# Kernel tuning notes

Hardware: AMD Instinct MI355X
Metric: run time of the kernel (lower is better)

The kernel has to match this reference:

```python
import jax, jax.numpy as jnp
import numpy as np

NODES, NFEAT = 128, 256


def setup_inputs() -> dict:
    key = jax.random.key(0)
    k1, k2, k3, k4, k5, k6 = jax.random.split(key, 6)
    B = 512
    x = jax.random.normal(k1, (B, NODES, NFEAT), dtype=jnp.float32)
    adj = jax.random.uniform(k2, (B, NODES, NODES), dtype=jnp.float32)
    # GraphConvolution(nfeat, nfeat): weight [nfeat, nfeat], bias [nfeat]
    s = 1.0 / np.sqrt(NFEAT)
    gcn_w = jax.random.uniform(k3, (NFEAT, NFEAT), minval=-s, maxval=s, dtype=jnp.float32)
    gcn_b = jax.random.uniform(k4, (NFEAT,), minval=-s, maxval=s, dtype=jnp.float32)
    # fc: Linear(nfeat*nodes, nfeat), torch layout [out, in]
    s2 = 1.0 / np.sqrt(NFEAT * NODES)
    fc_w = jax.random.uniform(k5, (NFEAT, NFEAT * NODES), minval=-s2, maxval=s2, dtype=jnp.float32)
    fc_b = jax.random.uniform(k6, (NFEAT,), minval=-s2, maxval=s2, dtype=jnp.float32)
    return {"x": x, "adj": adj, "gcn_w": gcn_w, "gcn_b": gcn_b, "fc_w": fc_w, "fc_b": fc_b}


def reference(x, adj, gcn_w, gcn_b, fc_w, fc_b):
    B = x.shape[0]
    # Per-sample loop GCN fused as batched matmuls:
    # support = X @ W ; out = A @ support + b
    support = jnp.einsum('bnf,fg->bng', x, gcn_w)          # [B, nodes, nfeat]
    mid = jnp.einsum('bnm,bmg->bng', adj, support) + gcn_b  # [B, nodes, nfeat]
    # cat along dim0 then reshape(-1, nfeat*nodes) == per-graph flatten
    flat = mid.reshape(B, NODES * NFEAT)
    output = flat @ fc_w.T + fc_b                           # [B, nfeat]
    useful_input = x[:, 0, :]                               # [B, nfeat]
    return (output, useful_input, output)
```

## Files before the change

kernel.cpp:

```cpp
#include <hip/hip_runtime.h>

#define NODES 128
#define NFEAT 256
#define BATCH 512
#define KTOT  (NODES * NFEAT)
#define SPLIT 64
#define KCH   (KTOT / SPLIT)

typedef __bf16 bf16_t;
typedef bf16_t bf16x4 __attribute__((ext_vector_type(4)));
typedef bf16_t bf16x8 __attribute__((ext_vector_type(8)));
typedef float  f32x4  __attribute__((ext_vector_type(4)));

#define BK    32
#define LDK   40
#define BK2   64
#define LDK2  72
#define TILE  128
#define GT    64

__device__ __forceinline__ void bar() {
    asm volatile("s_waitcnt lgkmcnt(0)\n\ts_barrier" ::: "memory");
}

__device__ __forceinline__ bf16x8 cvt8(const float4 a, const float4 b) {
    bf16x8 t;
    t[0] = (bf16_t)a.x; t[1] = (bf16_t)a.y; t[2] = (bf16_t)a.z; t[3] = (bf16_t)a.w;
    t[4] = (bf16_t)b.x; t[5] = (bf16_t)b.y; t[6] = (bf16_t)b.z; t[7] = (bf16_t)b.w;
    return t;
}

struct XT { float4 v[4]; };
__device__ __forceinline__ void xload(const float* __restrict__ src, int ld, int k0,
                                      int tid, XT& t) {
#pragma unroll
    for (int i = 0; i < 2; i++) {
        int f = tid + i * 256, r = f >> 2, c = f & 3;
        t.v[2 * i]     = *(const float4*)(src + (size_t)r * ld + k0 + c * 8);
        t.v[2 * i + 1] = *(const float4*)(src + (size_t)r * ld + k0 + c * 8 + 4);
    }
}
__device__ __forceinline__ void xstore(bf16_t* __restrict__ dst, int tid, const XT& t) {
#pragma unroll
    for (int i = 0; i < 2; i++) {
        int f = tid + i * 256, r = f >> 2, c = f & 3;
        *(bf16x8*)(dst + r * LDK + c * 8) = cvt8(t.v[2 * i], t.v[2 * i + 1]);
    }
}

struct XT2 { float4 v[8]; };
__device__ __forceinline__ void xload2(const float* __restrict__ src, int ld, int k0,
                                       int tid, XT2& t) {
#pragma unroll
    for (int i = 0; i < 4; i++) {
        int f = tid + i * 256, r = f >> 3, c = f & 7;
        t.v[2 * i]     = *(const float4*)(src + (size_t)r * ld + k0 + c * 8);
        t.v[2 * i + 1] = *(const float4*)(src + (size_t)r * ld + k0 + c * 8 + 4);
    }
}
__device__ __forceinline__ void xstore2(bf16_t* __restrict__ dst, int tid, const XT2& t) {
#pragma unroll
    for (int i = 0; i < 4; i++) {
        int f = tid + i * 256, r = f >> 3, c = f & 7;
        *(bf16x8*)(dst + r * LDK2 + c * 8) = cvt8(t.v[2 * i], t.v[2 * i + 1]);
    }
}

struct AT2 { bf16x8 v[4]; };
__device__ __forceinline__ void aload2(const bf16_t* __restrict__ src, int ld, int k0,
                                       int tid, AT2& t) {
#pragma unroll
    for (int i = 0; i < 4; i++) {
        int f = tid + i * 256, r = f >> 3, c = f & 7;
        t.v[i] = *(const bf16x8*)(src + (size_t)r * ld + k0 + c * 8);
    }
}
__device__ __forceinline__ void astore2(bf16_t* __restrict__ dst, int tid, const AT2& t) {
#pragma unroll
    for (int i = 0; i < 4; i++) {
        int f = tid + i * 256, r = f >> 3, c = f & 7;
        *(bf16x8*)(dst + r * LDK2 + c * 8) = t.v[i];
    }
}

__global__ __launch_bounds__(256)
void k_wt(const float* __restrict__ w, bf16_t* __restrict__ wT) {
    const int g0 = blockIdx.x * 4;
    const int k  = threadIdx.x;
    const float4 v = *(const float4*)(w + (size_t)k * NFEAT + g0);
    wT[(size_t)(g0 + 0) * NFEAT + k] = (bf16_t)v.x;
    wT[(size_t)(g0 + 1) * NFEAT + k] = (bf16_t)v.y;
    wT[(size_t)(g0 + 2) * NFEAT + k] = (bf16_t)v.z;
    wT[(size_t)(g0 + 3) * NFEAT + k] = (bf16_t)v.w;
}

__global__ __launch_bounds__(256)
void k_fwt(const float* __restrict__ w, bf16_t* __restrict__ wb) {
    const size_t i = ((size_t)blockIdx.x * 256 + threadIdx.x) * 8;
    const float4 a = *(const float4*)(w + i);
    const float4 b = *(const float4*)(w + i + 4);
    *(bf16x8*)(wb + i) = cvt8(a, b);
}

__global__ __launch_bounds__(256, 4)
void k_fused12(const float* __restrict__ x, const float* __restrict__ adj,
               const bf16_t* __restrict__ wT, const float* __restrict__ gcn_b,
               bf16_t* __restrict__ mid) {
    __shared__ __align__(16) bf16_t As[2][TILE * LDK];
    __shared__ __align__(16) bf16_t Sb[GT * 128];
    const int id  = blockIdx.y * 4 + blockIdx.x;
    const int xcd = id & 7, jj = id >> 3;
    const int b   = (xcd << 6) | (jj >> 2);
    const int n0  = (jj & 3) * GT;
    const int tid = threadIdx.x;
    const int lane = tid & 63, w = tid >> 6, wm = w & 1, wn = w >> 1;
    const int l15 = lane & 15, q = lane >> 4;
    const float* xb   = x   + (size_t)b * NODES * NFEAT;
    const float* adjb = adj + (size_t)b * NODES * NODES;

    const bf16_t* wrow[2];
#pragma unroll
    for (int j = 0; j < 2; j++)
        wrow[j] = wT + (size_t)(n0 + wn * 32 + j * 16 + l15) * NFEAT + q * 8;

    f32x4 acc[4][2] = {};
    {
        XT r[3];
        xload(xb, NFEAT, 0 * BK, tid, r[0]);
        xload(xb, NFEAT, 1 * BK, tid, r[1]);
        xload(xb, NFEAT, 2 * BK, tid, r[2]);
        xstore(As[0], tid, r[0]);
        bar();
#pragma unroll
        for (int k = 0; k < 8; k++) {
            if (k + 3 < 8) xload(xb, NFEAT, (k + 3) * BK, tid, r[k % 3]);
            bf16x8 bcur[2];
#pragma unroll
            for (int j = 0; j < 2; j++) bcur[j] = *(const bf16x8*)(wrow[j] + k * BK);
            bf16x8 a[4];
#pragma unroll
            for (int i = 0; i < 4; i++)
                a[i] = *(const bf16x8*)(&As[k & 1][(wm * 64 + i * 16 + l15) * LDK + q * 8]);
#pragma unroll
            for (int i = 0; i < 4; i++)
#pragma unroll
                for (int j = 0; j < 2; j++)
                    acc[i][j] = __builtin_amdgcn_mfma_f32_16x16x32_bf16(a[i], bcur[j], acc[i][j], 0, 0, 0);
            if (k + 1 < 8) xstore(As[(k + 1) & 1], tid, r[(k + 1) % 3]);
            bar();
        }
    }

    XT r[3];
    xload(adjb, NODES, 0 * BK, tid, r[0]);
    xload(adjb, NODES, 1 * BK, tid, r[1]);
    xload(adjb, NODES, 2 * BK, tid, r[2]);
#pragma unroll
    for (int i = 0; i < 4; i++)
#pragma unroll
        for (int j = 0; j < 2; j++)
#pragma unroll
            for (int rr = 0; rr < 4; rr++) {
                int m = wm * 64 + i * 16 + q * 4 + rr;
                int g = wn * 32 + j * 16 + l15;
                int slot = (m >> 3) ^ (g & 15);
                Sb[g * 128 + slot * 8 + (m & 7)] = (bf16_t)acc[i][j][rr];
            }
    bar();
    xstore(As[0], tid, r[0]);
    bar();

    f32x4 acc2[4][2] = {};
#pragma unroll
    for (int k = 0; k < 4; k++) {
        if (k + 3 < 4) xload(adjb, NODES, (k + 3) * BK, tid, r[k % 3]);
        bf16x8 a[4], bb[2];
#pragma unroll
        for (int i = 0; i < 4; i++)
            a[i] = *(const bf16x8*)(&As[k & 1][(wm * 64 + i * 16 + l15) * LDK + q * 8]);
#pragma unroll
        for (int j = 0; j < 2; j++) {
            int R = wn * 32 + j * 16 + l15;
            int slot = (k * 4 + q) ^ (R & 15);
            bb[j] = *(const bf16x8*)(&Sb[R * 128 + slot * 8]);
        }
#pragma unroll
        for (int i = 0; i < 4; i++)
#pragma unroll
            for (int j = 0; j < 2; j++)
                acc2[i][j] = __builtin_amdgcn_mfma_f32_16x16x32_bf16(a[i], bb[j], acc2[i][j], 0, 0, 0);
        if (k + 1 < 4) xstore(As[(k + 1) & 1], tid, r[(k + 1) % 3]);
        bar();
    }
    bf16_t* outb = mid + (size_t)b * NODES * NFEAT;
#pragma unroll
    for (int j = 0; j < 2; j++) {
        int g = n0 + wn * 32 + j * 16 + l15;
        float bias = gcn_b[g];
#pragma unroll
        for (int i = 0; i < 4; i++)
#pragma unroll
            for (int rr = 0; rr < 4; rr++) {
                int node = wm * 64 + i * 16 + q * 4 + rr;
                outb[(size_t)node * NFEAT + g] = (bf16_t)(acc2[i][j][rr] + bias);
            }
    }
}

__global__ __launch_bounds__(256, 2)
void k_out_bf(const bf16_t* __restrict__ flat, const bf16_t* __restrict__ fcwb,
              bf16_t* __restrict__ part) {
    __shared__ __align__(16) bf16_t As[2][TILE * LDK2];
    __shared__ __align__(16) bf16_t Bs[2][TILE * LDK2];
    const int m0 = blockIdx.x * TILE;
    const int n0 = blockIdx.y * TILE;
    const int kb = blockIdx.z * KCH;
    const int tid = threadIdx.x;
    const int lane = tid & 63, w = tid >> 6, wm = w & 1, wn = w >> 1;
    const int l15 = lane & 15, q = lane >> 4;
    f32x4 acc[4][4] = {};
    const bf16_t* fa = flat + (size_t)m0 * KTOT;
    const bf16_t* fb = fcwb + (size_t)n0 * KTOT;

    AT2 ra[3], rb[2];
    aload2(fa, KTOT, kb + 0 * BK2, tid, ra[0]);
    aload2(fb, KTOT, kb + 0 * BK2, tid, rb[0]);
    aload2(fa, KTOT, kb + 1 * BK2, tid, ra[1]);
    aload2(fb, KTOT, kb + 1 * BK2, tid, rb[1]);
    aload2(fa, KTOT, kb + 2 * BK2, tid, ra[2]);
    astore2(As[0], tid, ra[0]);
    astore2(Bs[0], tid, rb[0]);
    bar();
#pragma unroll
    for (int k = 0; k < 8; k++) {
        if (k + 3 < 8) aload2(fa, KTOT, kb + (k + 3) * BK2, tid, ra[k % 3]);
        if (k + 2 < 8) aload2(fb, KTOT, kb + (k + 2) * BK2, tid, rb[k & 1]);
#pragma unroll
        for (int kk = 0; kk < BK2; kk += BK) {
            bf16x8 a[4], bbf[4];
#pragma unroll
            for (int i = 0; i < 4; i++)
                a[i] = *(const bf16x8*)(&As[k & 1][(wm * 64 + i * 16 + l15) * LDK2 + kk + q * 8]);
#pragma unroll
            for (int j = 0; j < 4; j++)
                bbf[j] = *(const bf16x8*)(&Bs[k & 1][(wn * 64 + j * 16 + l15) * LDK2 + kk + q * 8]);
#pragma unroll
            for (int i = 0; i < 4; i++)
#pragma unroll
                for (int j = 0; j < 4; j++)
                    acc[i][j] = __builtin_amdgcn_mfma_f32_16x16x32_bf16(a[i], bbf[j], acc[i][j], 0, 0, 0);
        }
        if (k + 1 < 8) {
            astore2(As[(k + 1) & 1], tid, ra[(k + 1) % 3]);
            astore2(Bs[(k + 1) & 1], tid, rb[(k + 1) & 1]);
        }
        bar();
    }
    bf16_t* pb = part + (size_t)blockIdx.z * BATCH * NFEAT;
#pragma unroll
    for (int i = 0; i < 4; i++)
#pragma unroll
        for (int j = 0; j < 4; j++)
#pragma unroll
            for (int r = 0; r < 4; r++) {
                int bt_ = m0 + wm * 64 + i * 16 + q * 4 + r;
                int o   = n0 + wn * 64 + j * 16 + l15;
                pb[(size_t)bt_ * NFEAT + o] = (bf16_t)acc[i][j][r];
            }
}

__global__ __launch_bounds__(256, 2)
void k_out(const bf16_t* __restrict__ flat, const float* __restrict__ fcw,
           bf16_t* __restrict__ part) {
    __shared__ __align__(16) bf16_t As[2][TILE * LDK2];
    __shared__ __align__(16) bf16_t Bs[2][TILE * LDK2];
    const int m0 = blockIdx.x * TILE;
    const int n0 = blockIdx.y * TILE;
    const int kb = blockIdx.z * KCH;
    const int tid = threadIdx.x;
    const int lane = tid & 63, w = tid >> 6, wm = w & 1, wn = w >> 1;
    const int l15 = lane & 15, q = lane >> 4;
    f32x4 acc[4][4] = {};
    const bf16_t* fa = flat + (size_t)m0 * KTOT;
    const float*  fb = fcw + (size_t)n0 * KTOT;

    AT2 ra[3]; XT2 rb[2];
    aload2(fa, KTOT, kb + 0 * BK2, tid, ra[0]);
    xload2(fb, KTOT, kb + 0 * BK2, tid, rb[0]);
    aload2(fa, KTOT, kb + 1 * BK2, tid, ra[1]);
    xload2(fb, KTOT, kb + 1 * BK2, tid, rb[1]);
    aload2(fa, KTOT, kb + 2 * BK2, tid, ra[2]);
    astore2(As[0], tid, ra[0]);
    xstore2(Bs[0], tid, rb[0]);
    bar();
#pragma unroll
    for (int k = 0; k < 8; k++) {
        if (k + 3 < 8) aload2(fa, KTOT, kb + (k + 3) * BK2, tid, ra[k % 3]);
        if (k + 2 < 8) xload2(fb, KTOT, kb + (k + 2) * BK2, tid, rb[k & 1]);
#pragma unroll
        for (int kk = 0; kk < BK2; kk += BK) {
            bf16x8 a[4], bbf[4];
#pragma unroll
            for (int i = 0; i < 4; i++)
                a[i] = *(const bf16x8*)(&As[k & 1][(wm * 64 + i * 16 + l15) * LDK2 + kk + q * 8]);
#pragma unroll
            for (int j = 0; j < 4; j++)
                bbf[j] = *(const bf16x8*)(&Bs[k & 1][(wn * 64 + j * 16 + l15) * LDK2 + kk + q * 8]);
#pragma unroll
            for (int i = 0; i < 4; i++)
#pragma unroll
                for (int j = 0; j < 4; j++)
                    acc[i][j] = __builtin_amdgcn_mfma_f32_16x16x32_bf16(a[i], bbf[j], acc[i][j], 0, 0, 0);
        }
        if (k + 1 < 8) {
            astore2(As[(k + 1) & 1], tid, ra[(k + 1) % 3]);
            xstore2(Bs[(k + 1) & 1], tid, rb[(k + 1) & 1]);
        }
        bar();
    }
    bf16_t* pb = part + (size_t)blockIdx.z * BATCH * NFEAT;
#pragma unroll
    for (int i = 0; i < 4; i++)
#pragma unroll
        for (int j = 0; j < 4; j++)
#pragma unroll
            for (int r = 0; r < 4; r++) {
                int bt_ = m0 + wm * 64 + i * 16 + q * 4 + r;
                int o   = n0 + wn * 64 + j * 16 + l15;
                pb[(size_t)bt_ * NFEAT + o] = (bf16_t)acc[i][j][r];
            }
}

__global__ __launch_bounds__(256)
void k_reduce(const bf16_t* __restrict__ part, const float* __restrict__ fc_b,
              const float* __restrict__ x, float* __restrict__ out) {
    const int g4 = (blockIdx.x * 256 + threadIdx.x) * 4;
    const int o = g4 & (NFEAT - 1), b = g4 >> 8;
    float s[4];
    const float4 c0 = *(const float4*)(fc_b + o);
    s[0] = c0.x; s[1] = c0.y; s[2] = c0.z; s[3] = c0.w;
#pragma unroll 8
    for (int i = 0; i < SPLIT; i++) {
        bf16x4 p = *(const bf16x4*)(part + (size_t)i * BATCH * NFEAT + g4);
#pragma unroll
        for (int j = 0; j < 4; j++) s[j] += (float)p[j];
    }
    float4 o0 = make_float4(s[0], s[1], s[2], s[3]);
    *(float4*)(out + g4) = o0;
    *(float4*)(out + 2 * BATCH * NFEAT + g4) = o0;
    *(float4*)(out + BATCH * NFEAT + g4) = *(const float4*)(x + (size_t)b * NODES * NFEAT + o);
}

extern "C" void kernel_launch(void* const* d_in, const int* in_sizes, int n_in,
                              void* d_out, int out_size, void* d_ws, size_t ws_size,
                              hipStream_t stream) {
    const float* x     = (const float*)d_in[0];
    const float* adj   = (const float*)d_in[1];
    const float* gcn_w = (const float*)d_in[2];
    const float* gcn_b = (const float*)d_in[3];
    const float* fc_w  = (const float*)d_in[4];
    const float* fc_b  = (const float*)d_in[5];
    float* out = (float*)d_out;

    const size_t midB  = (size_t)BATCH * NODES * NFEAT * 2;
    const size_t partB = (size_t)SPLIT * BATCH * NFEAT * 2;
    const size_t fcwB  = (size_t)NFEAT * KTOT * 2;
    bf16_t* wT   = (bf16_t*)d_ws;
    bf16_t* mid  = (bf16_t*)((char*)d_ws + 131072);
    bf16_t* part = (bf16_t*)((char*)d_ws + 131072 + midB);
    bf16_t* fcwb = (bf16_t*)((char*)d_ws + 131072 + midB + partB);
    const bool cv = ws_size >= 131072 + midB + partB + fcwB;

    k_wt     <<<dim3(64), dim3(256), 0, stream>>>(gcn_w, wT);
    if (cv)
        k_fwt<<<dim3(4096), dim3(256), 0, stream>>>(fc_w, fcwb);
    k_fused12<<<dim3(4, BATCH), dim3(256), 0, stream>>>(x, adj, wT, gcn_b, mid);
    if (cv)
        k_out_bf<<<dim3(4, 2, SPLIT), dim3(256), 0, stream>>>(mid, fcwb, part);
    else
        k_out   <<<dim3(4, 2, SPLIT), dim3(256), 0, stream>>>(mid, fc_w, part);
    k_reduce <<<dim3(128), dim3(256), 0, stream>>>(part, fc_b, x, out);
}
```

Baseline: 213.1 us.

## Widen GCN tile to 128 cols, load A operands directly, merge fc_w conversion

The fused GCN kernel now gives each block 128 output columns instead of 64, so each batch needs 2 blocks instead of 4 and x/adj are re-read fewer times. The LDS staging of x and adj is dropped: each lane loads and converts its MFMA A fragments straight from global memory. The fc_w fp32-to-bf16 conversion is folded into the same launch as extra blocks, removing one kernel launch and letting it overlap with the GCN work. In exchange, accumulator register pressure doubles, global loads are less coalesced, and there is no software prefetch for the direct loads.

```diff
diff --git a/kernel.cpp b/kernel.cpp
--- a/kernel.cpp
+++ b/kernel.cpp
@@ -12,12 +12,11 @@
 typedef bf16_t bf16x8 __attribute__((ext_vector_type(8)));
 typedef float  f32x4  __attribute__((ext_vector_type(4)));
 
-#define BK    32
-#define LDK   40
 #define BK2   64
 #define LDK2  72
 #define TILE  128
-#define GT    64
+#define FUSED_BLOCKS 1024
+#define CONV_BLOCKS  2048
 
 __device__ __forceinline__ void bar() {
     asm volatile("s_waitcnt lgkmcnt(0)\n\ts_barrier" ::: "memory");
@@ -30,22 +29,10 @@
     return t;
 }
 
-struct XT { float4 v[4]; };
-__device__ __forceinline__ void xload(const float* __restrict__ src, int ld, int k0,
-                                      int tid, XT& t) {
-#pragma unroll
-    for (int i = 0; i < 2; i++) {
-        int f = tid + i * 256, r = f >> 2, c = f & 3;
-        t.v[2 * i]     = *(const float4*)(src + (size_t)r * ld + k0 + c * 8);
-        t.v[2 * i + 1] = *(const float4*)(src + (size_t)r * ld + k0 + c * 8 + 4);
-    }
-}
-__device__ __forceinline__ void xstore(bf16_t* __restrict__ dst, int tid, const XT& t) {
-#pragma unroll
-    for (int i = 0; i < 2; i++) {
-        int f = tid + i * 256, r = f >> 2, c = f & 3;
-        *(bf16x8*)(dst + r * LDK + c * 8) = cvt8(t.v[2 * i], t.v[2 * i + 1]);
-    }
+__device__ __forceinline__ bf16x8 ldcvt(const float* __restrict__ p) {
+    const float4 a = *(const float4*)p;
+    const float4 b = *(const float4*)(p + 4);
+    return cvt8(a, b);
 }
 
 struct XT2 { float4 v[8]; };
@@ -94,108 +81,94 @@
     wT[(size_t)(g0 + 3) * NFEAT + k] = (bf16_t)v.w;
 }
 
-__global__ __launch_bounds__(256)
-void k_fwt(const float* __restrict__ w, bf16_t* __restrict__ wb) {
-    const size_t i = ((size_t)blockIdx.x * 256 + threadIdx.x) * 8;
-    const float4 a = *(const float4*)(w + i);
-    const float4 b = *(const float4*)(w + i + 4);
-    *(bf16x8*)(wb + i) = cvt8(a, b);
-}
-
 __global__ __launch_bounds__(256, 4)
 void k_fused12(const float* __restrict__ x, const float* __restrict__ adj,
                const bf16_t* __restrict__ wT, const float* __restrict__ gcn_b,
-               bf16_t* __restrict__ mid) {
-    __shared__ __align__(16) bf16_t As[2][TILE * LDK];
-    __shared__ __align__(16) bf16_t Sb[GT * 128];
-    const int id  = blockIdx.y * 4 + blockIdx.x;
+               bf16_t* __restrict__ mid,
+               const float* __restrict__ fcw, bf16_t* __restrict__ fcwb) {
+    __shared__ __align__(16) bf16_t Sb[TILE * 128];
+
+    if (blockIdx.x >= FUSED_BLOCKS) {
+        const size_t base = ((size_t)(blockIdx.x - FUSED_BLOCKS) * 256 + threadIdx.x) * 16;
+        const float4 a0 = *(const float4*)(fcw + base);
+        const float4 a1 = *(const float4*)(fcw + base + 4);
+        const float4 a2 = *(const float4*)(fcw + base + 8);
+        const float4 a3 = *(const float4*)(fcw + base + 12);
+        *(bf16x8*)(fcwb + base)     = cvt8(a0, a1);
+        *(bf16x8*)(fcwb + base + 8) = cvt8(a2, a3);
+        return;
+    }
+
+    const int id  = blockIdx.x;
     const int xcd = id & 7, jj = id >> 3;
-    const int b   = (xcd << 6) | (jj >> 2);
-    const int n0  = (jj & 3) * GT;
+    const int b   = (xcd << 6) | (jj >> 1);
+    const int n0  = (jj & 1) * TILE;
     const int tid = threadIdx.x;
     const int lane = tid & 63, w = tid >> 6, wm = w & 1, wn = w >> 1;
     const int l15 = lane & 15, q = lane >> 4;
     const float* xb   = x   + (size_t)b * NODES * NFEAT;
     const float* adjb = adj + (size_t)b * NODES * NODES;
 
-    const bf16_t* wrow[2];
-#pragma unroll
-    for (int j = 0; j < 2; j++)
-        wrow[j] = wT + (size_t)(n0 + wn * 32 + j * 16 + l15) * NFEAT + q * 8;
-
-    f32x4 acc[4][2] = {};
+    f32x4 acc[4][4] = {};
     {
-        XT r[3];
-        xload(xb, NFEAT, 0 * BK, tid, r[0]);
-        xload(xb, NFEAT, 1 * BK, tid, r[1]);
-        xload(xb, NFEAT, 2 * BK, tid, r[2]);
-        xstore(As[0], tid, r[0]);
-        bar();
+        const float*  xa = xb + (size_t)(wm * 64 + l15) * NFEAT + q * 8;
+        const bf16_t* wp = wT + (size_t)(n0 + wn * 64 + l15) * NFEAT + q * 8;
 #pragma unroll
         for (int k = 0; k < 8; k++) {
-            if (k + 3 < 8) xload(xb, NFEAT, (k + 3) * BK, tid, r[k % 3]);
-            bf16x8 bcur[2];
-#pragma unroll
-            for (int j = 0; j < 2; j++) bcur[j] = *(const bf16x8*)(wrow[j] + k * BK);
-            bf16x8 a[4];
-#pragma unroll
-            for (int i = 0; i < 4; i++)
-                a[i] = *(const bf16x8*)(&As[k & 1][(wm * 64 + i * 16 + l15) * LDK + q * 8]);
-#pragma unroll
-            for (int i = 0; i < 4; i++)
-#pragma unroll
-                for (int j = 0; j < 2; j++)
-                    acc[i][j] = __builtin_amdgcn_mfma_f32_16x16x32_bf16(a[i], bcur[j], acc[i][j], 0, 0, 0);
-            if (k + 1 < 8) xstore(As[(k + 1) & 1], tid, r[(k + 1) % 3]);
-            bar();
-        }
-    }
-
-    XT r[3];
-    xload(adjb, NODES, 0 * BK, tid, r[0]);
-    xload(adjb, NODES, 1 * BK, tid, r[1]);
-    xload(adjb, NODES, 2 * BK, tid, r[2]);
+            bf16x8 bcur[4];
+#pragma unroll
+            for (int j = 0; j < 4; j++)
+                bcur[j] = *(const bf16x8*)(wp + (size_t)j * 16 * NFEAT + k * 32);
+#pragma unroll
+            for (int i = 0; i < 4; i++) {
+                bf16x8 af = ldcvt(xa + (size_t)i * 16 * NFEAT + k * 32);
+#pragma unroll
+                for (int j = 0; j < 4; j++)
+                    acc[i][j] = __builtin_amdgcn_mfma_f32_16x16x32_bf16(af, bcur[j], acc[i][j], 0, 0, 0);
+            }
+        }
+    }
+
 #pragma unroll
     for (int i = 0; i < 4; i++)
 #pragma unroll
-        for (int j = 0; j < 2; j++)
-#pragma unroll
-            for (int rr = 0; rr < 4; rr++) {
-                int m = wm * 64 + i * 16 + q * 4 + rr;
-                int g = wn * 32 + j * 16 + l15;
-                int slot = (m >> 3) ^ (g & 15);
-                Sb[g * 128 + slot * 8 + (m & 7)] = (bf16_t)acc[i][j][rr];
-            }
+        for (int j = 0; j < 4; j++) {
+            int m = wm * 64 + i * 16 + q * 4;
+            int g = wn * 64 + j * 16 + l15;
+            int slot = (m >> 3) ^ (g & 15);
+            bf16x4 v;
+            v[0] = (bf16_t)acc[i][j][0]; v[1] = (bf16_t)acc[i][j][1];
+            v[2] = (bf16_t)acc[i][j][2]; v[3] = (bf16_t)acc[i][j][3];
+            *(bf16x4*)(&Sb[g * 128 + slot * 8 + (m & 7)]) = v;
+        }
     bar();
-    xstore(As[0], tid, r[0]);
-    bar();
-
-    f32x4 acc2[4][2] = {};
-#pragma unroll
-    for (int k = 0; k < 4; k++) {
-        if (k + 3 < 4) xload(adjb, NODES, (k + 3) * BK, tid, r[k % 3]);
-        bf16x8 a[4], bb[2];
-#pragma unroll
-        for (int i = 0; i < 4; i++)
-            a[i] = *(const bf16x8*)(&As[k & 1][(wm * 64 + i * 16 + l15) * LDK + q * 8]);
-#pragma unroll
-        for (int j = 0; j < 2; j++) {
-            int R = wn * 32 + j * 16 + l15;
-            int slot = (k * 4 + q) ^ (R & 15);
-            bb[j] = *(const bf16x8*)(&Sb[R * 128 + slot * 8]);
-        }
-#pragma unroll
-        for (int i = 0; i < 4; i++)
-#pragma unroll
-            for (int j = 0; j < 2; j++)
-                acc2[i][j] = __builtin_amdgcn_mfma_f32_16x16x32_bf16(a[i], bb[j], acc2[i][j], 0, 0, 0);
-        if (k + 1 < 4) xstore(As[(k + 1) & 1], tid, r[(k + 1) % 3]);
-        bar();
-    }
+
+    f32x4 acc2[4][4] = {};
+    {
+        const float* aa = adjb + (size_t)(wm * 64 + l15) * NODES + q * 8;
+#pragma unroll
+        for (int k = 0; k < 4; k++) {
+            bf16x8 bb[4];
+#pragma unroll
+            for (int j = 0; j < 4; j++) {
+                int R = wn * 64 + j * 16 + l15;
+                int slot = (k * 4 + q) ^ (R & 15);
+                bb[j] = *(const bf16x8*)(&Sb[R * 128 + slot * 8]);
+            }
+#pragma unroll
+            for (int i = 0; i < 4; i++) {
+                bf16x8 af = ldcvt(aa + (size_t)i * 16 * NODES + k * 32);
+#pragma unroll
+                for (int j = 0; j < 4; j++)
+                    acc2[i][j] = __builtin_amdgcn_mfma_f32_16x16x32_bf16(af, bb[j], acc2[i][j], 0, 0, 0);
+            }
+        }
+    }
+
     bf16_t* outb = mid + (size_t)b * NODES * NFEAT;
 #pragma unroll
-    for (int j = 0; j < 2; j++) {
-        int g = n0 + wn * 32 + j * 16 + l15;
+    for (int j = 0; j < 4; j++) {
+        int g = n0 + wn * 64 + j * 16 + l15;
         float bias = gcn_b[g];
 #pragma unroll
         for (int i = 0; i < 4; i++)
@@ -236,7 +209,7 @@
         if (k + 3 < 8) aload2(fa, KTOT, kb + (k + 3) * BK2, tid, ra[k % 3]);
         if (k + 2 < 8) aload2(fb, KTOT, kb + (k + 2) * BK2, tid, rb[k & 1]);
 #pragma unroll
-        for (int kk = 0; kk < BK2; kk += BK) {
+        for (int kk = 0; kk < BK2; kk += 32) {
             bf16x8 a[4], bbf[4];
 #pragma unroll
             for (int i = 0; i < 4; i++)
@@ -298,7 +271,7 @@
         if (k + 3 < 8) aload2(fa, KTOT, kb + (k + 3) * BK2, tid, ra[k % 3]);
         if (k + 2 < 8) xload2(fb, KTOT, kb + (k + 2) * BK2, tid, rb[k & 1]);
 #pragma unroll
-        for (int kk = 0; kk < BK2; kk += BK) {
+        for (int kk = 0; kk < BK2; kk += 32) {
             bf16x8 a[4], bbf[4];
 #pragma unroll
             for (int i = 0; i < 4; i++)
@@ -372,9 +345,8 @@
     const bool cv = ws_size >= 131072 + midB + partB + fcwB;
 
     k_wt     <<<dim3(64), dim3(256), 0, stream>>>(gcn_w, wT);
-    if (cv)
-        k_fwt<<<dim3(4096), dim3(256), 0, stream>>>(fc_w, fcwb);
-    k_fused12<<<dim3(4, BATCH), dim3(256), 0, stream>>>(x, adj, wT, gcn_b, mid);
+    k_fused12<<<dim3(cv ? FUSED_BLOCKS + CONV_BLOCKS : FUSED_BLOCKS), dim3(256), 0, stream>>>(
+        x, adj, wT, gcn_b, mid, fc_w, fcwb);
     if (cv)
         k_out_bf<<<dim3(4, 2, SPLIT), dim3(256), 0, stream>>>(mid, fcwb, part);
     else
```

After: 228.9 us. 1.07x slower.
